# Performance work log

Measured on AMD Instinct MI355X. Metric: run time of the kernel, lower is better.

The kernel has to match this reference:

```python
import jax, jax.numpy as jnp
import numpy as np

B, S, H = 4, 256, 8
N_MB, N_C = 50000, 1000
P, BS, CS, L0, L1, L2 = 32, 16, 16, 96, 32, 16


def setup_inputs() -> dict:
    key = jax.random.key(0)
    ks = jax.random.split(key, 12)
    sd = 0.02
    return {
        "attention_scores": jax.random.normal(ks[0], (B, H, S, S), dtype=jnp.float32),
        "b_seq": jax.random.randint(ks[1], (B, S), 0, N_MB + 1, dtype=jnp.int32),
        "c_seq": jax.random.randint(ks[2], (B, S), 0, N_C + 2, dtype=jnp.int32),
        "e_pos": jax.random.normal(ks[3], (S * 2, H, P), dtype=jnp.float32) * sd,
        "e_bi": jax.random.normal(ks[4], (N_MB + 1, H, BS), dtype=jnp.float32) * sd,
        "e_bj": jax.random.normal(ks[5], (N_MB + 1, H, BS), dtype=jnp.float32) * sd,
        "e_ci": jax.random.normal(ks[6], (N_C + 2, H, CS), dtype=jnp.float32) * sd,
        "e_cj": jax.random.normal(ks[7], (N_C + 2, H, CS), dtype=jnp.float32) * sd,
        "w1_e": jax.random.normal(ks[8], (L0, L1, H), dtype=jnp.float32) * sd,
        "w2_e": jax.random.normal(ks[9], (L1, L2, H), dtype=jnp.float32) * sd,
        "w3_e": jax.random.normal(ks[10], (L2, H), dtype=jnp.float32) * sd,
    }


def reference(attention_scores, b_seq, c_seq, e_pos, e_bi, e_bj, e_ci, e_cj, w1_e, w2_e, w3_e):
    b, h, s, _ = attention_scores.shape
    pos = jnp.arange(s, dtype=jnp.int32)
    # relative position index (i - j + seq_len), shared across batch: [S,S]
    f_pos = pos[:, None] - pos[None, :] + s
    emb_pos = e_pos[f_pos]                 # [S,S,H,P]
    emb_bi = e_bi[b_seq]                   # [B,S,H,BS]
    emb_bj = e_bj[b_seq]
    emb_ci = e_ci[c_seq]                   # [B,S,H,CS]
    emb_cj = e_cj[c_seq]
    # concat of broadcasted features -> e: [B,S,S,H,L0]
    e = jnp.concatenate([
        jnp.broadcast_to(emb_pos[None], (b, s, s, h, emb_pos.shape[-1])),
        jnp.broadcast_to(emb_bi[:, :, None], (b, s, s, h, emb_bi.shape[-1])),
        jnp.broadcast_to(emb_bj[:, None, :], (b, s, s, h, emb_bj.shape[-1])),
        jnp.broadcast_to(emb_ci[:, :, None], (b, s, s, h, emb_ci.shape[-1])),
        jnp.broadcast_to(emb_cj[:, None, :], (b, s, s, h, emb_cj.shape[-1])),
    ], axis=-1)
    e1 = jax.nn.relu(jnp.einsum('bmnhd,dkh->bmnhk', e, w1_e))
    e2 = jax.nn.relu(jnp.einsum('bmnhk,klh->bmnhl', e1, w2_e))
    da_score = jnp.einsum('bmnhk,kh->bhmn', e2, w3_e)
    return attention_scores + da_score
```

## Files before the change

### kernel.cpp

```cpp
#include <hip/hip_runtime.h>
#include <stdint.h>

typedef __attribute__((ext_vector_type(8))) short short8;
typedef __attribute__((ext_vector_type(4))) float f32x4;

#define SEQ 256
#define NH 8

__device__ __forceinline__ uint32_t cvt_pk_bf16(float lo, float hi) {
  uint32_t r;
  asm("v_cvt_pk_bf16_f32 %0, %1, %2" : "=v"(r) : "v"(lo), "v"(hi));
  return r;
}

__device__ __forceinline__ short8 pack8(f32x4 a, f32x4 b) {
  union { uint32_t u[4]; short8 v; } t;
  t.u[0] = cvt_pk_bf16(a[0], a[1]);
  t.u[1] = cvt_pk_bf16(a[2], a[3]);
  t.u[2] = cvt_pk_bf16(b[0], b[1]);
  t.u[3] = cvt_pk_bf16(b[2], b[3]);
  return t.v;
}

__global__ __launch_bounds__(512, 4) void dis_att_fused(
    const float* __restrict__ attn, const int* __restrict__ bseq,
    const int* __restrict__ cseq, const float* __restrict__ epos,
    const float* __restrict__ ebi, const float* __restrict__ ebj,
    const float* __restrict__ eci, const float* __restrict__ ecj,
    const float* __restrict__ w1, const float* __restrict__ w2,
    const float* __restrict__ w3, float* __restrict__ out) {
  __shared__ float sW1[96][33];
  __shared__ float sAp[128][36];
  __shared__ float sAi[64][36];
  __shared__ float sAj[64][36];
  int tid = threadIdx.x;
  int wg = blockIdx.x;
  int nt = wg & 3, mt = (wg >> 2) & 3, h = (wg >> 4) & 7, b = wg >> 7;
  int m0 = mt * 64, n0 = nt * 64;
  int f0 = m0 - n0 + 193;
  int lane = tid & 63, w = tid >> 6;
  int lcol = lane & 15, kb = lane >> 4, k8 = kb * 8;
  f32x4 zero = {0.f, 0.f, 0.f, 0.f};

#pragma unroll
  for (int i = 0; i < 6; ++i) {
    int idx = tid + 512 * i;
    sW1[idx >> 5][idx & 31] = w1[(idx >> 5) * 256 + (idx & 31) * 8 + h];
  }
  {
    int r = tid >> 3, q = tid & 7;
#pragma unroll
    for (int p = 0; p < 2; ++p) {
      int row = r + 64 * p;
      int f = f0 + row; if (f > 511) f = 511;
      *(f32x4*)&sAp[row][q * 4] = *(const f32x4*)(epos + (f * NH + h) * 32 + q * 4);
    }
    int gmi = b * SEQ + m0 + r, gmj = b * SEQ + n0 + r;
    if (q < 4) {
      int bi = bseq[gmi], bj = bseq[gmj];
      *(f32x4*)&sAi[r][q * 4] = *(const f32x4*)(ebi + (bi * NH + h) * 16 + q * 4);
      *(f32x4*)&sAj[r][q * 4] = *(const f32x4*)(ebj + (bj * NH + h) * 16 + q * 4);
    } else {
      int ci = cseq[gmi], cj = cseq[gmj];
      *(f32x4*)&sAi[r][q * 4] = *(const f32x4*)(eci + (ci * NH + h) * 16 + (q - 4) * 4);
      *(f32x4*)&sAj[r][q * 4] = *(const f32x4*)(ecj + (cj * NH + h) * 16 + (q - 4) * 4);
    }
  }
  __syncthreads();

  short8 af[2], bf[2];
  if (w < 4) {
#pragma unroll
    for (int kt = 0; kt < 2; ++kt) {
      union { uint32_t u[4]; short8 v; } t;
#pragma unroll
      for (int r = 0; r < 4; ++r)
        t.u[r] = cvt_pk_bf16(sW1[k8 + 2 * r][kt * 16 + lcol],
                             sW1[k8 + 2 * r + 1][kt * 16 + lcol]);
      bf[kt] = t.v;
    }
#pragma unroll
    for (int t = 0; t < 2; ++t) {
      int row = (w + t * 4) * 16 + lcol;
      af[t] = pack8(*(const f32x4*)&sAp[row][k8],
                    *(const f32x4*)&sAp[row][k8 + 4]);
    }
  } else {
    int isI = w < 6;
    int p0 = isI ? ((kb < 2 ? 32 : 48) + k8)
                 : ((kb < 2 ? 48 : 64) + k8);
#pragma unroll
    for (int kt = 0; kt < 2; ++kt) {
      union { uint32_t u[4]; short8 v; } t;
#pragma unroll
      for (int r = 0; r < 4; ++r)
        t.u[r] = cvt_pk_bf16(sW1[p0 + 2 * r][kt * 16 + lcol],
                             sW1[p0 + 2 * r + 1][kt * 16 + lcol]);
      bf[kt] = t.v;
    }
    int w2_ = isI ? (w - 4) : (w - 6);
#pragma unroll
    for (int t = 0; t < 2; ++t) {
      int row = (w2_ * 2 + t) * 16 + lcol;
      const float* base = isI ? &sAi[row][0] : &sAj[row][0];
      af[t] = pack8(*(const f32x4*)(base + k8), *(const f32x4*)(base + k8 + 4));
    }
  }
  __syncthreads();

#pragma unroll
  for (int t = 0; t < 2; ++t) {
#pragma unroll
    for (int kt = 0; kt < 2; ++kt) {
      f32x4 d = __builtin_amdgcn_mfma_f32_16x16x32_bf16(af[t], bf[kt], zero, 0, 0, 0);
      if (w < 4) {
        int mt_ = w + t * 4;
#pragma unroll
        for (int r = 0; r < 4; ++r)
          sAp[mt_ * 16 + kb * 4 + r][kt * 16 + lcol] = d[r];
      } else {
        int isI = w < 6;
        int mt_ = (isI ? (w - 4) : (w - 6)) * 2 + t;
#pragma unroll
        for (int r = 0; r < 4; ++r) {
          float* T = isI ? &sAi[mt_ * 16 + kb * 4 + r][kt * 16 + lcol]
                         : &sAj[mt_ * 16 + kb * 4 + r][kt * 16 + lcol];
          *T = d[r];
        }
      }
    }
  }
  __syncthreads();

  union { uint32_t u[4]; short8 v; } w2f;
#pragma unroll
  for (int r = 0; r < 4; ++r) {
    float lo = w2[(k8 + 2 * r) * 128 + lcol * 8 + h];
    float hi = w2[(k8 + 2 * r + 1) * 128 + lcol * 8 + h];
    w2f.u[r] = cvt_pk_bf16(lo, hi);
  }
  float w3v[4];
#pragma unroll
  for (int r = 0; r < 4; ++r) w3v[r] = w3[(kb * 4 + r) * 8 + h];

  f32x4 ajA[4], ajB[4];
#pragma unroll
  for (int ng = 0; ng < 4; ++ng) {
    int nl = ng * 16 + lcol;
    ajA[ng] = *(const f32x4*)&sAj[nl][k8];
    ajB[ng] = *(const f32x4*)&sAj[nl][k8 + 4];
  }

  const float* attn_b = attn + (b * NH + h) * SEQ * SEQ;
  float* out_b = out + (b * NH + h) * SEQ * SEQ;
  int bit4 = kb & 1, bit5 = kb & 2;

#pragma unroll
  for (int s = 0; s < 2; ++s) {
    int mb = w * 8 + s * 4;
    float av[4];
    int idxs[4];
#pragma unroll
    for (int ng = 0; ng < 4; ++ng) {
      idxs[ng] = (m0 + mb + kb) * SEQ + n0 + ng * 16 + lcol;
      av[ng] = attn_b[idxs[ng]];
    }
    f32x4 aiA[4], aiB[4];
#pragma unroll
    for (int mi = 0; mi < 4; ++mi) {
      aiA[mi] = *(const f32x4*)&sAi[mb + mi][k8];
      aiB[mi] = *(const f32x4*)&sAi[mb + mi][k8 + 4];
    }
#pragma unroll
    for (int ng = 0; ng < 4; ++ng) {
      int nl = ng * 16 + lcol;
      f32x4 pA[4], pB[4];
#pragma unroll
      for (int mi = 0; mi < 4; ++mi) {
        int rl = mb + mi - nl + 63;
        pA[mi] = *(const f32x4*)&sAp[rl][k8];
        pB[mi] = *(const f32x4*)&sAp[rl][k8 + 4];
      }
      __builtin_amdgcn_sched_barrier(0);
      float part[4];
#pragma unroll
      for (int mi = 0; mi < 4; ++mi) {
        f32x4 s0 = pA[mi] + aiA[mi] + ajA[ng];
        f32x4 s1 = pB[mi] + aiB[mi] + ajB[ng];
        union { uint32_t u[4]; short8 v; } ef;
        ef.u[0] = cvt_pk_bf16(fmaxf(s0[0], 0.f), fmaxf(s0[1], 0.f));
        ef.u[1] = cvt_pk_bf16(fmaxf(s0[2], 0.f), fmaxf(s0[3], 0.f));
        ef.u[2] = cvt_pk_bf16(fmaxf(s1[0], 0.f), fmaxf(s1[1], 0.f));
        ef.u[3] = cvt_pk_bf16(fmaxf(s1[2], 0.f), fmaxf(s1[3], 0.f));
        f32x4 d = __builtin_amdgcn_mfma_f32_16x16x32_bf16(w2f.v, ef.v, zero, 0, 0, 0);
        part[mi] = fmaxf(d[0], 0.f) * w3v[0] + fmaxf(d[1], 0.f) * w3v[1] +
                   fmaxf(d[2], 0.f) * w3v[2] + fmaxf(d[3], 0.f) * w3v[3];
      }
      float mineA = bit4 ? part[1] : part[0];
      float sendA = bit4 ? part[0] : part[1];
      float mineB = bit4 ? part[3] : part[2];
      float sendB = bit4 ? part[2] : part[3];
      mineA += __shfl_xor(sendA, 16, 64);
      mineB += __shfl_xor(sendB, 16, 64);
      float keep = bit5 ? mineB : mineA;
      float send = bit5 ? mineA : mineB;
      float res = keep + __shfl_xor(send, 32, 64);
      out_b[idxs[ng]] = av[ng] + res;
    }
  }
}

extern "C" void kernel_launch(void* const* d_in, const int* in_sizes, int n_in,
                              void* d_out, int out_size, void* d_ws, size_t ws_size,
                              hipStream_t stream) {
  const float* attn = (const float*)d_in[0];
  const int* bseq   = (const int*)d_in[1];
  const int* cseq   = (const int*)d_in[2];
  const float* epos = (const float*)d_in[3];
  const float* ebi  = (const float*)d_in[4];
  const float* ebj  = (const float*)d_in[5];
  const float* eci  = (const float*)d_in[6];
  const float* ecj  = (const float*)d_in[7];
  const float* w1   = (const float*)d_in[8];
  const float* w2   = (const float*)d_in[9];
  const float* w3   = (const float*)d_in[10];
  float* out = (float*)d_out;

  hipLaunchKernelGGL(dis_att_fused, dim3(512), dim3(512), 0, stream,
                     attn, bseq, cseq, epos, ebi, ebj, eci, ecj, w1, w2, w3, out);
}
```

Measured before the change: 22.10 us.

## Store layer-1 partials as packed fp16 and do add/relu with packed math

Converts W1 and the embedding tiles to packed bf16 in shared memory during staging, so MFMA operand fragments load directly without per-use conversion. Stores the first-layer MFMA outputs as packed fp16 pairs via lane shuffles, then in the hot loop sums and ReLUs them with v_pk_add_f16/v_pk_max_f16 and feeds an fp16 MFMA for layer 2. This halves LDS footprint and read traffic and cuts VALU conversions, allowing higher occupancy (launch bounds raised to 8). It trades away fp32 accumulation of the layer-1 sum for fp16 precision with round-toward-zero conversion.

```diff
diff --git a/kernel.cpp b/kernel.cpp
--- a/kernel.cpp
+++ b/kernel.cpp
@@ -2,7 +2,10 @@
 #include <stdint.h>
 
 typedef __attribute__((ext_vector_type(8))) short short8;
+typedef __attribute__((ext_vector_type(8))) _Float16 half8;
 typedef __attribute__((ext_vector_type(4))) float f32x4;
+typedef __attribute__((ext_vector_type(4))) uint32_t u32x4;
+typedef __attribute__((ext_vector_type(2))) uint32_t u32x2;
 
 #define SEQ 256
 #define NH 8
@@ -12,40 +15,48 @@
   asm("v_cvt_pk_bf16_f32 %0, %1, %2" : "=v"(r) : "v"(lo), "v"(hi));
   return r;
 }
-
-__device__ __forceinline__ short8 pack8(f32x4 a, f32x4 b) {
-  union { uint32_t u[4]; short8 v; } t;
-  t.u[0] = cvt_pk_bf16(a[0], a[1]);
-  t.u[1] = cvt_pk_bf16(a[2], a[3]);
-  t.u[2] = cvt_pk_bf16(b[0], b[1]);
-  t.u[3] = cvt_pk_bf16(b[2], b[3]);
-  return t.v;
-}
-
-__global__ __launch_bounds__(512, 4) void dis_att_fused(
+__device__ __forceinline__ uint32_t cvt_pk_f16(float lo, float hi) {
+  uint32_t r;
+  asm("v_cvt_pkrtz_f16_f32 %0, %1, %2" : "=v"(r) : "v"(lo), "v"(hi));
+  return r;
+}
+__device__ __forceinline__ uint32_t pk_add(uint32_t a, uint32_t b) {
+  uint32_t r;
+  asm("v_pk_add_f16 %0, %1, %2" : "=v"(r) : "v"(a), "v"(b));
+  return r;
+}
+__device__ __forceinline__ uint32_t pk_relu(uint32_t a) {
+  uint32_t r;
+  asm("v_pk_max_f16 %0, %1, 0" : "=v"(r) : "v"(a));
+  return r;
+}
+
+__global__ __launch_bounds__(512, 8) void dis_att_fused(
     const float* __restrict__ attn, const int* __restrict__ bseq,
     const int* __restrict__ cseq, const float* __restrict__ epos,
     const float* __restrict__ ebi, const float* __restrict__ ebj,
     const float* __restrict__ eci, const float* __restrict__ ecj,
     const float* __restrict__ w1, const float* __restrict__ w2,
     const float* __restrict__ w3, float* __restrict__ out) {
-  __shared__ float sW1[96][33];
-  __shared__ float sAp[128][36];
-  __shared__ float sAi[64][36];
-  __shared__ float sAj[64][36];
+  __shared__ uint32_t sW1p[48][33];
+  __shared__ uint32_t tAp[128][20];
+  __shared__ uint32_t tAi[64][20];
+  __shared__ uint32_t tAj[64][20];
   int tid = threadIdx.x;
   int wg = blockIdx.x;
   int nt = wg & 3, mt = (wg >> 2) & 3, h = (wg >> 4) & 7, b = wg >> 7;
   int m0 = mt * 64, n0 = nt * 64;
   int f0 = m0 - n0 + 193;
   int lane = tid & 63, w = tid >> 6;
-  int lcol = lane & 15, kb = lane >> 4, k8 = kb * 8;
+  int lcol = lane & 15, kb = lane >> 4, k8 = kb * 8, kq = kb * 4;
   f32x4 zero = {0.f, 0.f, 0.f, 0.f};
 
 #pragma unroll
-  for (int i = 0; i < 6; ++i) {
+  for (int i = 0; i < 3; ++i) {
     int idx = tid + 512 * i;
-    sW1[idx >> 5][idx & 31] = w1[(idx >> 5) * 256 + (idx & 31) * 8 + h];
+    int pp = idx >> 5, c = idx & 31;
+    sW1p[pp][c] = cvt_pk_bf16(w1[(2 * pp) * 256 + c * 8 + h],
+                              w1[(2 * pp + 1) * 256 + c * 8 + h]);
   }
   {
     int r = tid >> 3, q = tid & 7;
@@ -53,103 +64,94 @@
     for (int p = 0; p < 2; ++p) {
       int row = r + 64 * p;
       int f = f0 + row; if (f > 511) f = 511;
-      *(f32x4*)&sAp[row][q * 4] = *(const f32x4*)(epos + (f * NH + h) * 32 + q * 4);
+      f32x4 v = *(const f32x4*)(epos + (f * NH + h) * 32 + q * 4);
+      u32x2 o = {cvt_pk_bf16(v[0], v[1]), cvt_pk_bf16(v[2], v[3])};
+      *(u32x2*)&tAp[row][q * 2] = o;
     }
     int gmi = b * SEQ + m0 + r, gmj = b * SEQ + n0 + r;
     if (q < 4) {
       int bi = bseq[gmi], bj = bseq[gmj];
-      *(f32x4*)&sAi[r][q * 4] = *(const f32x4*)(ebi + (bi * NH + h) * 16 + q * 4);
-      *(f32x4*)&sAj[r][q * 4] = *(const f32x4*)(ebj + (bj * NH + h) * 16 + q * 4);
+      f32x4 vi = *(const f32x4*)(ebi + (bi * NH + h) * 16 + q * 4);
+      f32x4 vj = *(const f32x4*)(ebj + (bj * NH + h) * 16 + q * 4);
+      u32x2 oi = {cvt_pk_bf16(vi[0], vi[1]), cvt_pk_bf16(vi[2], vi[3])};
+      u32x2 oj = {cvt_pk_bf16(vj[0], vj[1]), cvt_pk_bf16(vj[2], vj[3])};
+      *(u32x2*)&tAi[r][q * 2] = oi;
+      *(u32x2*)&tAj[r][q * 2] = oj;
     } else {
       int ci = cseq[gmi], cj = cseq[gmj];
-      *(f32x4*)&sAi[r][q * 4] = *(const f32x4*)(eci + (ci * NH + h) * 16 + (q - 4) * 4);
-      *(f32x4*)&sAj[r][q * 4] = *(const f32x4*)(ecj + (cj * NH + h) * 16 + (q - 4) * 4);
+      f32x4 vi = *(const f32x4*)(eci + (ci * NH + h) * 16 + (q - 4) * 4);
+      f32x4 vj = *(const f32x4*)(ecj + (cj * NH + h) * 16 + (q - 4) * 4);
+      u32x2 oi = {cvt_pk_bf16(vi[0], vi[1]), cvt_pk_bf16(vi[2], vi[3])};
+      u32x2 oj = {cvt_pk_bf16(vj[0], vj[1]), cvt_pk_bf16(vj[2], vj[3])};
+      *(u32x2*)&tAi[r][8 + (q - 4) * 2] = oi;
+      *(u32x2*)&tAj[r][8 + (q - 4) * 2] = oj;
     }
   }
   __syncthreads();
 
+  int isI = w < 6;
+  int w2_ = isI ? (w - 4) : (w - 6);
+  int p0h = (w < 4) ? kq
+                    : (isI ? ((kb < 2 ? 16 : 24) + kq)
+                           : ((kb < 2 ? 24 : 32) + kq));
   short8 af[2], bf[2];
-  if (w < 4) {
-#pragma unroll
-    for (int kt = 0; kt < 2; ++kt) {
-      union { uint32_t u[4]; short8 v; } t;
-#pragma unroll
-      for (int r = 0; r < 4; ++r)
-        t.u[r] = cvt_pk_bf16(sW1[k8 + 2 * r][kt * 16 + lcol],
-                             sW1[k8 + 2 * r + 1][kt * 16 + lcol]);
-      bf[kt] = t.v;
-    }
-#pragma unroll
-    for (int t = 0; t < 2; ++t) {
-      int row = (w + t * 4) * 16 + lcol;
-      af[t] = pack8(*(const f32x4*)&sAp[row][k8],
-                    *(const f32x4*)&sAp[row][k8 + 4]);
-    }
-  } else {
-    int isI = w < 6;
-    int p0 = isI ? ((kb < 2 ? 32 : 48) + k8)
-                 : ((kb < 2 ? 48 : 64) + k8);
-#pragma unroll
-    for (int kt = 0; kt < 2; ++kt) {
-      union { uint32_t u[4]; short8 v; } t;
-#pragma unroll
-      for (int r = 0; r < 4; ++r)
-        t.u[r] = cvt_pk_bf16(sW1[p0 + 2 * r][kt * 16 + lcol],
-                             sW1[p0 + 2 * r + 1][kt * 16 + lcol]);
-      bf[kt] = t.v;
-    }
-    int w2_ = isI ? (w - 4) : (w - 6);
-#pragma unroll
-    for (int t = 0; t < 2; ++t) {
-      int row = (w2_ * 2 + t) * 16 + lcol;
-      const float* base = isI ? &sAi[row][0] : &sAj[row][0];
-      af[t] = pack8(*(const f32x4*)(base + k8), *(const f32x4*)(base + k8 + 4));
-    }
+#pragma unroll
+  for (int kt = 0; kt < 2; ++kt) {
+    union { uint32_t u[4]; short8 v; } t;
+#pragma unroll
+    for (int r = 0; r < 4; ++r) t.u[r] = sW1p[p0h + r][kt * 16 + lcol];
+    bf[kt] = t.v;
+  }
+#pragma unroll
+  for (int t = 0; t < 2; ++t) {
+    int row = ((w < 4) ? (w + t * 4) : (w2_ * 2 + t)) * 16 + lcol;
+    const uint32_t* base = (w < 4) ? &tAp[row][0]
+                                   : (isI ? &tAi[row][0] : &tAj[row][0]);
+    union { u32x4 u; short8 v; } t2;
+    t2.u = *(const u32x4*)(base + kq);
+    af[t] = t2.v;
   }
   __syncthreads();
 
 #pragma unroll
   for (int t = 0; t < 2; ++t) {
+    int row_base = ((w < 4) ? (w + t * 4) : (w2_ * 2 + t)) * 16;
 #pragma unroll
     for (int kt = 0; kt < 2; ++kt) {
       f32x4 d = __builtin_amdgcn_mfma_f32_16x16x32_bf16(af[t], bf[kt], zero, 0, 0, 0);
-      if (w < 4) {
-        int mt_ = w + t * 4;
-#pragma unroll
-        for (int r = 0; r < 4; ++r)
-          sAp[mt_ * 16 + kb * 4 + r][kt * 16 + lcol] = d[r];
-      } else {
-        int isI = w < 6;
-        int mt_ = (isI ? (w - 4) : (w - 6)) * 2 + t;
+      f32x4 dn;
+#pragma unroll
+      for (int r = 0; r < 4; ++r) dn[r] = __shfl_xor(d[r], 1, 64);
+      if ((lcol & 1) == 0) {
+        int pcol = kt * 8 + (lcol >> 1);
 #pragma unroll
         for (int r = 0; r < 4; ++r) {
-          float* T = isI ? &sAi[mt_ * 16 + kb * 4 + r][kt * 16 + lcol]
-                         : &sAj[mt_ * 16 + kb * 4 + r][kt * 16 + lcol];
-          *T = d[r];
+          uint32_t pk = cvt_pk_f16(d[r], dn[r]);
+          int prow = row_base + kb * 4 + r;
+          if (w < 4)    tAp[prow][pcol] = pk;
+          else if (isI) tAi[prow][pcol] = pk;
+          else          tAj[prow][pcol] = pk;
         }
       }
     }
   }
   __syncthreads();
 
-  union { uint32_t u[4]; short8 v; } w2f;
+  union { uint32_t u[4]; half8 v; } w2f;
 #pragma unroll
   for (int r = 0; r < 4; ++r) {
     float lo = w2[(k8 + 2 * r) * 128 + lcol * 8 + h];
     float hi = w2[(k8 + 2 * r + 1) * 128 + lcol * 8 + h];
-    w2f.u[r] = cvt_pk_bf16(lo, hi);
+    w2f.u[r] = cvt_pk_f16(lo, hi);
   }
   float w3v[4];
 #pragma unroll
   for (int r = 0; r < 4; ++r) w3v[r] = w3[(kb * 4 + r) * 8 + h];
 
-  f32x4 ajA[4], ajB[4];
-#pragma unroll
-  for (int ng = 0; ng < 4; ++ng) {
-    int nl = ng * 16 + lcol;
-    ajA[ng] = *(const f32x4*)&sAj[nl][k8];
-    ajB[ng] = *(const f32x4*)&sAj[nl][k8 + 4];
-  }
+  u32x4 ajP[4];
+#pragma unroll
+  for (int ng = 0; ng < 4; ++ng)
+    ajP[ng] = *(const u32x4*)&tAj[ng * 16 + lcol][kq];
 
   const float* attn_b = attn + (b * NH + h) * SEQ * SEQ;
   float* out_b = out + (b * NH + h) * SEQ * SEQ;
@@ -165,34 +167,26 @@
       idxs[ng] = (m0 + mb + kb) * SEQ + n0 + ng * 16 + lcol;
       av[ng] = attn_b[idxs[ng]];
     }
-    f32x4 aiA[4], aiB[4];
-#pragma unroll
-    for (int mi = 0; mi < 4; ++mi) {
-      aiA[mi] = *(const f32x4*)&sAi[mb + mi][k8];
-      aiB[mi] = *(const f32x4*)&sAi[mb + mi][k8 + 4];
-    }
+    u32x4 aiP[4];
+#pragma unroll
+    for (int mi = 0; mi < 4; ++mi)
+      aiP[mi] = *(const u32x4*)&tAi[mb + mi][kq];
 #pragma unroll
     for (int ng = 0; ng < 4; ++ng) {
       int nl = ng * 16 + lcol;
-      f32x4 pA[4], pB[4];
-#pragma unroll
-      for (int mi = 0; mi < 4; ++mi) {
-        int rl = mb + mi - nl + 63;
-        pA[mi] = *(const f32x4*)&sAp[rl][k8];
-        pB[mi] = *(const f32x4*)&sAp[rl][k8 + 4];
-      }
+      u32x4 pP[4];
+#pragma unroll
+      for (int mi = 0; mi < 4; ++mi)
+        pP[mi] = *(const u32x4*)&tAp[mb + mi - nl + 63][kq];
       __builtin_amdgcn_sched_barrier(0);
       float part[4];
 #pragma unroll
       for (int mi = 0; mi < 4; ++mi) {
-        f32x4 s0 = pA[mi] + aiA[mi] + ajA[ng];
-        f32x4 s1 = pB[mi] + aiB[mi] + ajB[ng];
-        union { uint32_t u[4]; short8 v; } ef;
-        ef.u[0] = cvt_pk_bf16(fmaxf(s0[0], 0.f), fmaxf(s0[1], 0.f));
-        ef.u[1] = cvt_pk_bf16(fmaxf(s0[2], 0.f), fmaxf(s0[3], 0.f));
-        ef.u[2] = cvt_pk_bf16(fmaxf(s1[0], 0.f), fmaxf(s1[1], 0.f));
-        ef.u[3] = cvt_pk_bf16(fmaxf(s1[2], 0.f), fmaxf(s1[3], 0.f));
-        f32x4 d = __builtin_amdgcn_mfma_f32_16x16x32_bf16(w2f.v, ef.v, zero, 0, 0, 0);
+        union { uint32_t u[4]; half8 v; } ef;
+#pragma unroll
+        for (int r = 0; r < 4; ++r)
+          ef.u[r] = pk_relu(pk_add(pk_add(pP[mi][r], aiP[mi][r]), ajP[ng][r]));
+        f32x4 d = __builtin_amdgcn_mfma_f32_16x16x32_f16(w2f.v, ef.v, zero, 0, 0, 0);
         part[mi] = fmaxf(d[0], 0.f) * w3v[0] + fmaxf(d[1], 0.f) * w3v[1] +
                    fmaxf(d[2], 0.f) * w3v[2] + fmaxf(d[3], 0.f) * w3v[3];
       }
```

After: 25.09 us. 1.13x slower.

## Halve row tile to 32 and double grid, redistribute first-layer MFMA tasks

Applied to the files above, without the earlier changes.

Each workgroup now covers 32 query rows instead of 64, so the grid grows from 512 to 1024 workgroups and each wave handles one 4-row strip instead of two. Shared buffers for position and i-side projections shrink. The first-layer projection is rewritten as a list of 12 tile tasks spread over 8 waves, which drops one barrier. The aim is more parallelism and better load balance across CUs, paid for with more redundant staging of j-side and position embeddings and the weight loads per output.

```diff
diff --git a/kernel.cpp b/kernel.cpp
--- a/kernel.cpp
+++ b/kernel.cpp
@@ -30,13 +30,13 @@
     const float* __restrict__ w1, const float* __restrict__ w2,
     const float* __restrict__ w3, float* __restrict__ out) {
   __shared__ float sW1[96][33];
-  __shared__ float sAp[128][36];
-  __shared__ float sAi[64][36];
+  __shared__ float sAp[96][36];
+  __shared__ float sAi[32][36];
   __shared__ float sAj[64][36];
   int tid = threadIdx.x;
   int wg = blockIdx.x;
-  int nt = wg & 3, mt = (wg >> 2) & 3, h = (wg >> 4) & 7, b = wg >> 7;
-  int m0 = mt * 64, n0 = nt * 64;
+  int nt = wg & 3, mt = (wg >> 2) & 7, h = (wg >> 5) & 7, b = wg >> 8;
+  int m0 = mt * 32, n0 = nt * 64;
   int f0 = m0 - n0 + 193;
   int lane = tid & 63, w = tid >> 6;
   int lcol = lane & 15, kb = lane >> 4, k8 = kb * 8;
@@ -49,83 +49,69 @@
   }
   {
     int r = tid >> 3, q = tid & 7;
-#pragma unroll
-    for (int p = 0; p < 2; ++p) {
-      int row = r + 64 * p;
-      int f = f0 + row; if (f > 511) f = 511;
-      *(f32x4*)&sAp[row][q * 4] = *(const f32x4*)(epos + (f * NH + h) * 32 + q * 4);
-    }
-    int gmi = b * SEQ + m0 + r, gmj = b * SEQ + n0 + r;
+    {
+      int f = f0 + r; if (f > 511) f = 511;
+      *(f32x4*)&sAp[r][q * 4] = *(const f32x4*)(epos + (f * NH + h) * 32 + q * 4);
+      if (r < 32) {
+        int f2 = f0 + 64 + r; if (f2 > 511) f2 = 511;
+        *(f32x4*)&sAp[64 + r][q * 4] =
+            *(const f32x4*)(epos + (f2 * NH + h) * 32 + q * 4);
+      }
+    }
+    int gmj = b * SEQ + n0 + r;
     if (q < 4) {
-      int bi = bseq[gmi], bj = bseq[gmj];
-      *(f32x4*)&sAi[r][q * 4] = *(const f32x4*)(ebi + (bi * NH + h) * 16 + q * 4);
+      int bj = bseq[gmj];
       *(f32x4*)&sAj[r][q * 4] = *(const f32x4*)(ebj + (bj * NH + h) * 16 + q * 4);
     } else {
-      int ci = cseq[gmi], cj = cseq[gmj];
-      *(f32x4*)&sAi[r][q * 4] = *(const f32x4*)(eci + (ci * NH + h) * 16 + (q - 4) * 4);
+      int cj = cseq[gmj];
       *(f32x4*)&sAj[r][q * 4] = *(const f32x4*)(ecj + (cj * NH + h) * 16 + (q - 4) * 4);
     }
+    if (r < 32) {
+      int gmi = b * SEQ + m0 + r;
+      if (q < 4) {
+        int bi = bseq[gmi];
+        *(f32x4*)&sAi[r][q * 4] = *(const f32x4*)(ebi + (bi * NH + h) * 16 + q * 4);
+      } else {
+        int ci = cseq[gmi];
+        *(f32x4*)&sAi[r][q * 4] = *(const f32x4*)(eci + (ci * NH + h) * 16 + (q - 4) * 4);
+      }
+    }
   }
   __syncthreads();
 
-  short8 af[2], bf[2];
-  if (w < 4) {
-#pragma unroll
-    for (int kt = 0; kt < 2; ++kt) {
-      union { uint32_t u[4]; short8 v; } t;
-#pragma unroll
-      for (int r = 0; r < 4; ++r)
-        t.u[r] = cvt_pk_bf16(sW1[k8 + 2 * r][kt * 16 + lcol],
-                             sW1[k8 + 2 * r + 1][kt * 16 + lcol]);
-      bf[kt] = t.v;
-    }
-#pragma unroll
-    for (int t = 0; t < 2; ++t) {
-      int row = (w + t * 4) * 16 + lcol;
-      af[t] = pack8(*(const f32x4*)&sAp[row][k8],
-                    *(const f32x4*)&sAp[row][k8 + 4]);
-    }
-  } else {
-    int isI = w < 6;
-    int p0 = isI ? ((kb < 2 ? 32 : 48) + k8)
-                 : ((kb < 2 ? 48 : 64) + k8);
-#pragma unroll
-    for (int kt = 0; kt < 2; ++kt) {
-      union { uint32_t u[4]; short8 v; } t;
-#pragma unroll
-      for (int r = 0; r < 4; ++r)
-        t.u[r] = cvt_pk_bf16(sW1[p0 + 2 * r][kt * 16 + lcol],
-                             sW1[p0 + 2 * r + 1][kt * 16 + lcol]);
-      bf[kt] = t.v;
-    }
-    int w2_ = isI ? (w - 4) : (w - 6);
-#pragma unroll
-    for (int t = 0; t < 2; ++t) {
-      int row = (w2_ * 2 + t) * 16 + lcol;
-      const float* base = isI ? &sAi[row][0] : &sAj[row][0];
-      af[t] = pack8(*(const f32x4*)(base + k8), *(const f32x4*)(base + k8 + 4));
-    }
-  }
-  __syncthreads();
-
-#pragma unroll
-  for (int t = 0; t < 2; ++t) {
-#pragma unroll
-    for (int kt = 0; kt < 2; ++kt) {
-      f32x4 d = __builtin_amdgcn_mfma_f32_16x16x32_bf16(af[t], bf[kt], zero, 0, 0, 0);
-      if (w < 4) {
-        int mt_ = w + t * 4;
+#pragma unroll
+  for (int tt = 0; tt < 2; ++tt) {
+    int task = w + tt * 8;
+    if (task < 12) {
+      int type = task < 6 ? 0 : (task < 8 ? 1 : 2);
+      int tile = task < 6 ? task : (task < 8 ? task - 6 : task - 8);
+      int p0 = (type == 0) ? k8
+             : (type == 1) ? ((kb < 2 ? 32 : 48) + k8)
+                           : ((kb < 2 ? 48 : 64) + k8);
+      short8 bf[2];
+#pragma unroll
+      for (int kt = 0; kt < 2; ++kt) {
+        union { uint32_t u[4]; short8 v; } t;
 #pragma unroll
         for (int r = 0; r < 4; ++r)
-          sAp[mt_ * 16 + kb * 4 + r][kt * 16 + lcol] = d[r];
-      } else {
-        int isI = w < 6;
-        int mt_ = (isI ? (w - 4) : (w - 6)) * 2 + t;
+          t.u[r] = cvt_pk_bf16(sW1[p0 + 2 * r][kt * 16 + lcol],
+                               sW1[p0 + 2 * r + 1][kt * 16 + lcol]);
+        bf[kt] = t.v;
+      }
+      int arow = tile * 16 + lcol;
+      const float* base = (type == 0) ? &sAp[arow][0]
+                        : (type == 1) ? &sAi[arow][0] : &sAj[arow][0];
+      short8 af = pack8(*(const f32x4*)(base + k8),
+                        *(const f32x4*)(base + k8 + 4));
+#pragma unroll
+      for (int kt = 0; kt < 2; ++kt) {
+        f32x4 d = __builtin_amdgcn_mfma_f32_16x16x32_bf16(af, bf[kt], zero, 0, 0, 0);
 #pragma unroll
         for (int r = 0; r < 4; ++r) {
-          float* T = isI ? &sAi[mt_ * 16 + kb * 4 + r][kt * 16 + lcol]
-                         : &sAj[mt_ * 16 + kb * 4 + r][kt * 16 + lcol];
-          *T = d[r];
+          int prow = tile * 16 + kb * 4 + r, pcol = kt * 16 + lcol;
+          if (type == 0)      sAp[prow][pcol] = d[r];
+          else if (type == 1) sAi[prow][pcol] = d[r];
+          else                sAj[prow][pcol] = d[r];
         }
       }
     }
@@ -155,9 +141,8 @@
   float* out_b = out + (b * NH + h) * SEQ * SEQ;
   int bit4 = kb & 1, bit5 = kb & 2;
 
-#pragma unroll
-  for (int s = 0; s < 2; ++s) {
-    int mb = w * 8 + s * 4;
+  {
+    int mb = w * 4;
     float av[4];
     int idxs[4];
 #pragma unroll
@@ -226,6 +211,6 @@
   const float* w3   = (const float*)d_in[10];
   float* out = (float*)d_out;
 
-  hipLaunchKernelGGL(dis_att_fused, dim3(512), dim3(512), 0, stream,
+  hipLaunchKernelGGL(dis_att_fused, dim3(1024), dim3(512), 0, stream,
                      attn, bseq, cseq, epos, ebi, ebj, eci, ecj, w1, w2, w3, out);
 }
```

After: 27.43 us. 24.1% more time.

## Pre-transpose W1 in a separate kernel and drop its shared-memory staging

Applied to the files above, without the earlier changes.

Adds a small kernel that reorders W1 into a per-head, per-output-column layout in workspace. The main kernel then loads its B fragments straight from global memory as contiguous vectors, removing the strided per-block W1 gather and the 12.7KB sW1 shared array. It also raises the launch-bounds occupancy hint from 4 to 8. The cost is an extra kernel launch and a dependency between the two kernels.

```diff
diff --git a/kernel.cpp b/kernel.cpp
--- a/kernel.cpp
+++ b/kernel.cpp
@@ -22,14 +22,22 @@
   return t.v;
 }
 
-__global__ __launch_bounds__(512, 4) void dis_att_fused(
+__global__ __launch_bounds__(256) void transpose_w1(
+    const float* __restrict__ w1, float* __restrict__ w1t) {
+  int t = blockIdx.x * 256 + threadIdx.x;
+  int p = t % 96;
+  int k = (t / 96) & 31;
+  int h = t / 3072;
+  w1t[t] = w1[p * 256 + k * 8 + h];
+}
+
+__global__ __launch_bounds__(512, 8) void dis_att_fused(
     const float* __restrict__ attn, const int* __restrict__ bseq,
     const int* __restrict__ cseq, const float* __restrict__ epos,
     const float* __restrict__ ebi, const float* __restrict__ ebj,
     const float* __restrict__ eci, const float* __restrict__ ecj,
-    const float* __restrict__ w1, const float* __restrict__ w2,
+    const float* __restrict__ w1t, const float* __restrict__ w2,
     const float* __restrict__ w3, float* __restrict__ out) {
-  __shared__ float sW1[96][33];
   __shared__ float sAp[128][36];
   __shared__ float sAi[64][36];
   __shared__ float sAj[64][36];
@@ -42,11 +50,6 @@
   int lcol = lane & 15, kb = lane >> 4, k8 = kb * 8;
   f32x4 zero = {0.f, 0.f, 0.f, 0.f};
 
-#pragma unroll
-  for (int i = 0; i < 6; ++i) {
-    int idx = tid + 512 * i;
-    sW1[idx >> 5][idx & 31] = w1[(idx >> 5) * 256 + (idx & 31) * 8 + h];
-  }
   {
     int r = tid >> 3, q = tid & 7;
 #pragma unroll
@@ -66,45 +69,29 @@
       *(f32x4*)&sAj[r][q * 4] = *(const f32x4*)(ecj + (cj * NH + h) * 16 + (q - 4) * 4);
     }
   }
+
+  short8 bf[2];
+  {
+    int p0 = (w < 4) ? k8
+           : ((w < 6) ? ((kb < 2 ? 32 : 48) + k8)
+                      : ((kb < 2 ? 48 : 64) + k8));
+#pragma unroll
+    for (int kt = 0; kt < 2; ++kt) {
+      const float* wrow = w1t + h * 3072 + (kt * 16 + lcol) * 96 + p0;
+      bf[kt] = pack8(*(const f32x4*)wrow, *(const f32x4*)(wrow + 4));
+    }
+  }
   __syncthreads();
 
-  short8 af[2], bf[2];
-  if (w < 4) {
-#pragma unroll
-    for (int kt = 0; kt < 2; ++kt) {
-      union { uint32_t u[4]; short8 v; } t;
-#pragma unroll
-      for (int r = 0; r < 4; ++r)
-        t.u[r] = cvt_pk_bf16(sW1[k8 + 2 * r][kt * 16 + lcol],
-                             sW1[k8 + 2 * r + 1][kt * 16 + lcol]);
-      bf[kt] = t.v;
-    }
-#pragma unroll
-    for (int t = 0; t < 2; ++t) {
-      int row = (w + t * 4) * 16 + lcol;
-      af[t] = pack8(*(const f32x4*)&sAp[row][k8],
-                    *(const f32x4*)&sAp[row][k8 + 4]);
-    }
-  } else {
-    int isI = w < 6;
-    int p0 = isI ? ((kb < 2 ? 32 : 48) + k8)
-                 : ((kb < 2 ? 48 : 64) + k8);
-#pragma unroll
-    for (int kt = 0; kt < 2; ++kt) {
-      union { uint32_t u[4]; short8 v; } t;
-#pragma unroll
-      for (int r = 0; r < 4; ++r)
-        t.u[r] = cvt_pk_bf16(sW1[p0 + 2 * r][kt * 16 + lcol],
-                             sW1[p0 + 2 * r + 1][kt * 16 + lcol]);
-      bf[kt] = t.v;
-    }
-    int w2_ = isI ? (w - 4) : (w - 6);
-#pragma unroll
-    for (int t = 0; t < 2; ++t) {
-      int row = (w2_ * 2 + t) * 16 + lcol;
-      const float* base = isI ? &sAi[row][0] : &sAj[row][0];
-      af[t] = pack8(*(const f32x4*)(base + k8), *(const f32x4*)(base + k8 + 4));
-    }
+  short8 af[2];
+  int isI = w < 6;
+  int w2_ = isI ? (w - 4) : (w - 6);
+#pragma unroll
+  for (int t = 0; t < 2; ++t) {
+    int row = ((w < 4) ? (w + t * 4) : (w2_ * 2 + t)) * 16 + lcol;
+    const float* base = (w < 4) ? &sAp[row][0]
+                                : (isI ? &sAi[row][0] : &sAj[row][0]);
+    af[t] = pack8(*(const f32x4*)(base + k8), *(const f32x4*)(base + k8 + 4));
   }
   __syncthreads();
 
@@ -119,8 +106,7 @@
         for (int r = 0; r < 4; ++r)
           sAp[mt_ * 16 + kb * 4 + r][kt * 16 + lcol] = d[r];
       } else {
-        int isI = w < 6;
-        int mt_ = (isI ? (w - 4) : (w - 6)) * 2 + t;
+        int mt_ = w2_ * 2 + t;
 #pragma unroll
         for (int r = 0; r < 4; ++r) {
           float* T = isI ? &sAi[mt_ * 16 + kb * 4 + r][kt * 16 + lcol]
@@ -226,6 +212,9 @@
   const float* w3   = (const float*)d_in[10];
   float* out = (float*)d_out;
 
+  float* w1t = (float*)d_ws;
+
+  hipLaunchKernelGGL(transpose_w1, dim3(96), dim3(256), 0, stream, w1, w1t);
   hipLaunchKernelGGL(dis_att_fused, dim3(512), dim3(512), 0, stream,
-                     attn, bseq, cseq, epos, ebi, ebj, eci, ecj, w1, w2, w3, out);
-}
+                     attn, bseq, cseq, epos, ebi, ebj, eci, ecj, w1t, w2, w3, out);
+}
```

New measurement: 79.22 us. +258.4%, slower.
